# Performance work log

Hardware: AMD Instinct MI355X
Metric: run time of the kernel (lower is better)

## Reference

```python
import jax, jax.numpy as jnp
import numpy as np

COST_W = {'cls': 1.0, 'center': 0.0, 'obj_ness': 0.0, 'giou': 2.0}
IOU_THRES = 0.25
MAX_DYN = 10
EPS = 1e-6
N_PRED, N_GT, N_CLS = 65536, 128, 256


def _to_bbox(centers, sizes):
    # center/size -> (x1,y1,z1,x2,y2,z2)
    return jnp.concatenate([centers - sizes / 2.0, centers + sizes / 2.0], axis=-1)


def _giou_3d(b1, b2):
    # b1 [N,6], b2 [M,6] -> giou [N,M] (axis_aligned_bbox_overlaps_3d, mode='giou')
    vol1 = jnp.prod(b1[:, 3:] - b1[:, :3], axis=-1)  # [N]
    vol2 = jnp.prod(b2[:, 3:] - b2[:, :3], axis=-1)  # [M]
    lt = jnp.maximum(b1[:, None, :3], b2[None, :, :3])  # [N,M,3]
    rb = jnp.minimum(b1[:, None, 3:], b2[None, :, 3:])
    overlap = jnp.prod(jnp.clip(rb - lt, 0.0), axis=-1)  # [N,M]
    union = jnp.maximum(vol1[:, None] + vol2[None, :] - overlap, EPS)
    iou = overlap / union
    elt = jnp.minimum(b1[:, None, :3], b2[None, :, :3])
    erb = jnp.maximum(b1[:, None, 3:], b2[None, :, 3:])
    enclose = jnp.maximum(jnp.prod(jnp.clip(erb - elt, 0.0), axis=-1), EPS)
    return iou - (enclose - union) / enclose


def _lsa(cost):
    # Jonker-Volgenant shortest-augmenting-path LAP (same optimum as
    # scipy.optimize.linear_sum_assignment). cost [n, m], n <= m.
    # Returns col4row[n]: column matched to each row.
    n, m = cost.shape
    u = np.zeros(n, np.float64)
    v = np.zeros(m, np.float64)
    col4row = np.full(n, -1, np.int64)
    row4col = np.full(m, -1, np.int64)
    cost = cost.astype(np.float64)
    for cur in range(n):
        shortest = np.full(m, np.inf)
        path = np.full(m, -1, np.int64)
        SC = np.zeros(m, bool)
        SR = []
        i, min_val, sink = cur, 0.0, -1
        while sink == -1:
            SR.append(i)
            r = min_val + cost[i] - u[i] - v
            upd = (~SC) & (r < shortest)
            shortest = np.where(upd, r, shortest)
            path = np.where(upd, i, path)
            masked = np.where(SC, np.inf, shortest)
            j = int(masked.argmin())
            min_val = masked[j]
            SC[j] = True
            if row4col[j] == -1:
                sink = j
            else:
                i = int(row4col[j])
        u[cur] += min_val
        for i2 in SR:
            if i2 != cur:
                u[i2] += min_val - shortest[col4row[i2]]
        v[SC] -= min_val - shortest[SC]
        j = sink
        while True:
            i2 = int(path[j])
            row4col[j] = i2
            col4row[i2], j = j, col4row[i2]
            if i2 == cur:
                break
    return col4row


def _dynamic_assign(giou, used0, order):
    # Sequential greedy IoU-threshold assignment over gts (ascending max-iou).
    NEG = jnp.float32(-1e9)
    n_pred = giou.shape[0]

    def step(used, gt_idx):
        col = giou[:, gt_idx]
        vals = jnp.where((col > IOU_THRES) & (~used), col, NEG)
        topv, topi = jax.lax.top_k(vals, MAX_DYN)
        valid = topv > NEG
        used = used | jnp.zeros((n_pred,), bool).at[topi].set(valid)
        return used, (jnp.where(valid, topi, -1), jnp.where(valid, gt_idx, -1))

    _, (dp, dg) = jax.lax.scan(step, used0, order)
    return dp.reshape(-1), dg.reshape(-1)  # padded with -1 where invalid


def setup_inputs() -> dict:
    key = jax.random.key(0)
    k = jax.random.split(key, 7)
    return {
        'all_centers': jax.random.normal(k[0], (N_PRED, 3), jnp.float32),
        'all_sizes': jax.random.uniform(k[1], (N_PRED, 3), jnp.float32),
        'all_cls': jax.random.normal(k[2], (N_PRED, N_CLS), jnp.float32),
        'all_objness': jax.random.normal(k[3], (N_PRED,), jnp.float32),
        'gt_centers': jax.random.normal(k[4], (N_GT, 3), jnp.float32),
        'gt_sizes': jax.random.uniform(k[5], (N_GT, 3), jnp.float32),
        'gt_labels': jax.random.randint(k[6], (N_GT,), 0, N_CLS, jnp.int64),
    }


def reference(all_centers, all_sizes, all_cls, all_objness, gt_centers, gt_sizes, gt_labels):
    pred_bbox = _to_bbox(all_centers, all_sizes)
    gt_bbox = _to_bbox(gt_centers, gt_sizes)
    giou = _giou_3d(pred_bbox, gt_bbox)  # [N, M]
    cost_class = -jax.nn.sigmoid(all_cls)[:, gt_labels]  # [N, M]
    cost_center = jnp.sum(jnp.abs(all_centers[:, None, :] - gt_centers[None, :, :]), axis=-1)  # cdist p=1
    cost_obj = -jax.nn.sigmoid(all_objness)[:, None]  # [N, 1]
    total_cost = (COST_W['cls'] * cost_class + COST_W['center'] * cost_center
                  + COST_W['obj_ness'] * cost_obj + COST_W['giou'] * (-giou))
    # Hungarian on transposed cost (M <= N): same optimal pairing as scipy on [N, M].
    col4row = _lsa(np.asarray(jax.device_get(total_cost)).T)
    pred_indices = jnp.asarray(col4row, jnp.int64)       # matched pred per gt
    gt_indices = jnp.arange(gt_labels.shape[0], dtype=jnp.int64)
    used0 = jnp.zeros((giou.shape[0],), bool).at[pred_indices].set(True)
    order = jnp.argsort(jnp.max(giou, axis=0))
    dp, dg = _dynamic_assign(giou, used0, order)
    combined_preds = jnp.concatenate([pred_indices, dp.astype(jnp.int64)])
    combined_gts = jnp.concatenate([gt_indices, dg.astype(jnp.int64)])
    return combined_preds, combined_gts
```

## Files before the change

### kernel.cpp

```cpp
#include <hip/hip_runtime.h>
#include <hip/hip_bf16.h>
#include <math.h>

#define NPRED 65536
#define NGT   128
#define NCLS  256
#define CAP   12288
#define VCAP  160
#define VSLOT 129
#define NLIST 129
#define LSTRIDE 132
#define KEEP  2048
#define KMIN  1418
#define GSPLIT 4
#define GPB   (NGT / GSPLIT)
#define SENT_I 0x7FFFFFFF


__device__ __forceinline__ unsigned f2u(float f) {
    unsigned u = __float_as_uint(f);
    return (u & 0x80000000u) ? ~u : (u | 0x80000000u);
}
__device__ __forceinline__ float u2f(unsigned x) {
    unsigned u = (x & 0x80000000u) ? (x ^ 0x80000000u) : ~x;
    return __uint_as_float(u);
}
__device__ __forceinline__ unsigned long long d2u(double d) {
    unsigned long long u = (unsigned long long)__double_as_longlong(d);
    return (u & 0x8000000000000000ull) ? ~u : (u | 0x8000000000000000ull);
}
__device__ __forceinline__ double u2d(unsigned long long x) {
    unsigned long long u = (x & 0x8000000000000000ull) ? (x ^ 0x8000000000000000ull) : ~x;
    return __longlong_as_double((long long)u);
}

__device__ __forceinline__ float giou3d(
    float pl0, float pl1, float pl2, float ph0, float ph1, float ph2, float pvol,
    float gl0, float gl1, float gl2, float gh0, float gh1, float gh2, float gvol)
{
#pragma clang fp contract(off)
    float c0 = fmaxf(fminf(ph0, gh0) - fmaxf(pl0, gl0), 0.0f);
    float c1 = fmaxf(fminf(ph1, gh1) - fmaxf(pl1, gl1), 0.0f);
    float c2 = fmaxf(fminf(ph2, gh2) - fmaxf(pl2, gl2), 0.0f);
    float overlap = (c0 * c1) * c2;
    float uni = fmaxf((pvol + gvol) - overlap, 1e-6f);
    float iou = overlap / uni;
    float e0 = fmaxf(fmaxf(ph0, gh0) - fminf(pl0, gl0), 0.0f);
    float e1 = fmaxf(fmaxf(ph1, gh1) - fminf(pl1, gl1), 0.0f);
    float e2 = fmaxf(fmaxf(ph2, gh2) - fminf(pl2, gl2), 0.0f);
    float enc = fmaxf((e0 * e1) * e2, 1e-6f);
    return iou - (enc - uni) / enc;
}


__global__ __launch_bounds__(256) void k_gather(
    const float* __restrict__ cls, const int* __restrict__ lab,
    float* __restrict__ costT,
    int* __restrict__ ccnt, unsigned* __restrict__ cmax, int* __restrict__ failFlag)
{
#pragma clang fp contract(off)
    __shared__ float tile[64][NCLS + 1];
    __shared__ int labl[NGT];
    int tid = threadIdx.x;
    int p0 = blockIdx.x * 64;
    if (blockIdx.x == 0) {
        if (tid < NGT) { ccnt[tid] = 0; cmax[tid] = 0u; }
        if (tid == 0) *failFlag = 0;
    }
    if (tid < NGT) labl[tid] = lab[tid];
    for (int it = 0; it < 16; ++it) {
        int row = it * 4 + (tid >> 6);
        int col = (tid & 63) * 4;
        const float4 v = *(const float4*)&cls[(size_t)(p0 + row) * NCLS + col];
        tile[row][col + 0] = v.x; tile[row][col + 1] = v.y;
        tile[row][col + 2] = v.z; tile[row][col + 3] = v.w;
    }
    __syncthreads();
    int lane = tid & 63;
    for (int rep = 0; rep < 32; ++rep) {
        int g = rep * 4 + (tid >> 6);
        float val = tile[lane][labl[g]];
        double s = 1.0 / (1.0 + exp(-(double)val));
        costT[(size_t)g * NPRED + p0 + lane] = -(float)s;
    }
}

__global__ __launch_bounds__(256) void k_cost(
    const float* __restrict__ pc, const float* __restrict__ ps,
    const float* __restrict__ gc, const float* __restrict__ gs,
    float* __restrict__ costT, int* __restrict__ ccnt, unsigned* __restrict__ cmax,
    int2* __restrict__ cpair)
{
#pragma clang fp contract(off)
    __shared__ float gb[GPB][6];
    __shared__ float gvol[GPB];
    __shared__ unsigned smax[GPB];
    __shared__ int cntl[GPB], basel[GPB], curl[GPB];
    int tid = threadIdx.x;
    int lane = tid & 63;
    int g0 = (blockIdx.x & (GSPLIT - 1)) * GPB;
    int p  = (blockIdx.x >> 2) * 256 + tid;

    if (tid < GPB) {
        int g = g0 + tid;
        float c0 = gc[g * 3 + 0], c1 = gc[g * 3 + 1], c2 = gc[g * 3 + 2];
        float s0 = gs[g * 3 + 0], s1 = gs[g * 3 + 1], s2 = gs[g * 3 + 2];
        float l0 = c0 - s0 / 2.0f, l1 = c1 - s1 / 2.0f, l2 = c2 - s2 / 2.0f;
        float h0 = c0 + s0 / 2.0f, h1 = c1 + s1 / 2.0f, h2 = c2 + s2 / 2.0f;
        gb[tid][0] = l0; gb[tid][1] = l1; gb[tid][2] = l2;
        gb[tid][3] = h0; gb[tid][4] = h1; gb[tid][5] = h2;
        gvol[tid] = ((h0 - l0) * (h1 - l1)) * (h2 - l2);
        smax[tid] = 0u; cntl[tid] = 0; curl[tid] = 0;
    }
    __syncthreads();

    float c0 = pc[p * 3 + 0], c1 = pc[p * 3 + 1], c2 = pc[p * 3 + 2];
    float s0 = ps[p * 3 + 0], s1 = ps[p * 3 + 1], s2 = ps[p * 3 + 2];
    float pl0 = c0 - s0 / 2.0f, pl1 = c1 - s1 / 2.0f, pl2 = c2 - s2 / 2.0f;
    float ph0 = c0 + s0 / 2.0f, ph1 = c1 + s1 / 2.0f, ph2 = c2 + s2 / 2.0f;
    float pvol = ((ph0 - pl0) * (ph1 - pl1)) * (ph2 - pl2);

    float gior[GPB];

#pragma unroll
    for (int gg = 0; gg < GPB; ++gg) {
        float gio = giou3d(pl0, pl1, pl2, ph0, ph1, ph2, pvol,
                           gb[gg][0], gb[gg][1], gb[gg][2], gb[gg][3], gb[gg][4], gb[gg][5],
                           gvol[gg]);
        gior[gg] = gio;
        float m = gio;
        for (int off = 32; off; off >>= 1) m = fmaxf(m, __shfl_xor(m, off, 64));
        unsigned long long mask = __ballot(gio > 0.25f);
        if (lane == 0) {
            atomicMax(&smax[gg], f2u(m));
            atomicAdd(&cntl[gg], __popcll(mask));
        }
        size_t ij = (size_t)(g0 + gg) * NPRED + p;
        float ns = costT[ij];
        costT[ij] = ns + (2.0f * (-gio));
    }
    __syncthreads();
    if (tid < GPB) {
        atomicMax(&cmax[g0 + tid], smax[tid]);
        basel[tid] = atomicAdd(&ccnt[g0 + tid], cntl[tid]);
    }
    __syncthreads();

#pragma unroll
    for (int gg = 0; gg < GPB; ++gg) {
        float gio = gior[gg];
        bool cand = (gio > 0.25f);
        unsigned long long mask = __ballot(cand);
        int cnt = __popcll(mask);
        int wo = 0;
        if (lane == 0 && cnt) wo = atomicAdd(&curl[gg], cnt);
        wo = __shfl(wo, 0, 64);
        if (cand) {
            int slot = basel[gg] + wo + __popcll(mask & ((1ull << lane) - 1ull));
            if (slot < CAP)
                cpair[(size_t)(g0 + gg) * CAP + slot] = make_int2(p, __float_as_int(gio));
        }
    }
}

__global__ __launch_bounds__(256) void k_toprow(
    const float* __restrict__ costT, int2* __restrict__ rowlist,
    const unsigned* __restrict__ cmax, int* __restrict__ order)
{
    __shared__ unsigned long long keys[2048];
    __shared__ int hist[256];
    __shared__ unsigned long long sh_prefix;
    __shared__ int sh_rank, sh_cnt, sh_ok;
    __shared__ unsigned msort[NGT];
    int tid = threadIdx.x;
    int row = blockIdx.x;

    if (row == NGT) {
        if (tid < NGT) msort[tid] = cmax[tid];
        __syncthreads();
        if (tid < NGT) {
            unsigned mt = msort[tid];
            int r = 0;
            for (int k = 0; k < NGT; ++k) {
                unsigned mk = msort[k];
                if (mk < mt || (mk == mt && k < tid)) r++;
            }
            order[r] = tid;
        }
        return;
    }
    const float* crow = costT + (size_t)row * NPRED;

    unsigned long long lv[8];
#pragma unroll
    for (int q = 0; q < 8; ++q) lv[q] = ~0ull;
    const float4* crow4 = (const float4*)crow;
    for (int it = tid; it < NPRED / 4; it += 256) {
        float4 v4 = crow4[it];
        int j = it * 4;
        float vv[4] = {v4.x, v4.y, v4.z, v4.w};
#pragma unroll
        for (int e = 0; e < 4; ++e) {
            unsigned long long key =
                ((unsigned long long)f2u(vv[e]) << 32) | (unsigned)(j + e);
            if (key < lv[7]) {
                unsigned long long c = key;
#pragma unroll
                for (int q = 0; q < 8; ++q) {
                    unsigned long long mx = (c > lv[q]) ? c : lv[q];
                    unsigned long long mn = (c > lv[q]) ? lv[q] : c;
                    lv[q] = mn; c = mx;
                }
            }
        }
    }
#pragma unroll
    for (int q = 0; q < 8; ++q) keys[tid * 8 + q] = lv[q];
    if (tid == 0) sh_ok = 1;
    __syncthreads();

    for (int k = 2; k <= 2048; k <<= 1) {
        for (int j2 = k >> 1; j2 > 0; j2 >>= 1) {
            for (int i = tid; i < 2048; i += 256) {
                int ixj = i ^ j2;
                if (ixj > i) {
                    unsigned long long a = keys[i], b2 = keys[ixj];
                    bool up = ((i & k) == 0);
                    if ((up && a > b2) || (!up && a < b2)) { keys[i] = b2; keys[ixj] = a; }
                }
            }
            __syncthreads();
        }
    }

    unsigned long long thr = keys[NLIST - 1];
    if (lv[7] < thr) sh_ok = 0;
    __syncthreads();

    if (sh_ok) {
        if (tid < NLIST) {
            unsigned long long key = keys[tid];
            rowlist[row * LSTRIDE + tid] =
                make_int2(__float_as_int(u2f((unsigned)(key >> 32))),
                          (int)(unsigned)(key & 0xFFFFFFFFull));
        }
        return;
    }

    if (tid == 0) { sh_prefix = 0ull; sh_rank = NLIST - 1; sh_cnt = 0; }
    __syncthreads();
    for (int d = 7; d >= 0; --d) {
        hist[tid] = 0;
        __syncthreads();
        unsigned long long pref = sh_prefix;
        int sh = (d + 1) * 8;
        for (int j = tid; j < NPRED; j += 256) {
            unsigned long long key = ((unsigned long long)f2u(crow[j]) << 32) | (unsigned)j;
            bool match = (sh >= 64) || ((key >> sh) == (pref >> sh));
            if (match) atomicAdd(&hist[(int)((key >> (d * 8)) & 255ull)], 1);
        }
        __syncthreads();
        if (tid == 0) {
            int rank = sh_rank, cum = 0, b = 0;
            for (; b < 256; ++b) { if (cum + hist[b] > rank) break; cum += hist[b]; }
            sh_prefix = pref | ((unsigned long long)b << (d * 8));
            sh_rank = rank - cum;
        }
        __syncthreads();
    }
    unsigned long long thr2 = sh_prefix;
    for (int j = tid; j < NPRED; j += 256) {
        unsigned long long key = ((unsigned long long)f2u(crow[j]) << 32) | (unsigned)j;
        if (key <= thr2) { int s = atomicAdd(&sh_cnt, 1); keys[s] = key; }
    }
    __syncthreads();
    if (tid >= sh_cnt) keys[tid] = ~0ull;
    __syncthreads();
    for (int k = 2; k <= 256; k <<= 1) {
        for (int j2 = k >> 1; j2 > 0; j2 >>= 1) {
            int i = tid, ixj = i ^ j2;
            if (ixj > i) {
                unsigned long long a = keys[i], b2 = keys[ixj];
                bool up = ((i & k) == 0);
                if ((up && a > b2) || (!up && a < b2)) { keys[i] = b2; keys[ixj] = a; }
            }
            __syncthreads();
        }
    }
    if (tid < NLIST) {
        unsigned long long key = keys[tid];
        rowlist[row * LSTRIDE + tid] =
            make_int2(__float_as_int(u2f((unsigned)(key >> 32))),
                      (int)(unsigned)(key & 0xFFFFFFFFull));
    }
}

__global__ __launch_bounds__(64) void k_lsa_sparse(
    const float* __restrict__ costT, const int2* __restrict__ rowlist,
    int* __restrict__ failFlag,
    unsigned* __restrict__ usedbits, int* __restrict__ out)
{
#pragma clang fp contract(off)
    __shared__ float  costV[NGT][VSLOT];
    __shared__ double u_l[NGT];
    __shared__ int    c4r[NGT];
    __shared__ int    slot4row[NGT];
    __shared__ int    headpos[NGT];
    __shared__ int    colidV[VCAP];
    __shared__ int    pathV[VCAP], r4cV[VCAP];
    __shared__ int    SRr[VCAP];
    __shared__ double headv[VCAP];
    __shared__ int    headj[VCAP];
    __shared__ unsigned vbits[2048];

    int lane = threadIdx.x;
    for (int w = lane; w < 2048; w += 64) vbits[w] = 0u;
    for (int r = lane; r < NGT; r += 64) {
        u_l[r] = 0.0; c4r[r] = -1; slot4row[r] = -1; headpos[r] = 0;
    }
    double short0 = INFINITY, short1 = INFINITY;
    double v0 = 0.0, v1 = 0.0;
    int col0 = SENT_I, col1 = SENT_I;
    int sc0 = 0, sc1 = 0;
    int nV = 0;
    bool fail = false;
    __syncthreads();

    for (int cur = 0; cur < NGT; ++cur) {
        short0 = INFINITY; short1 = INFINITY; sc0 = 0; sc1 = 0;
        if (lane < nV)      pathV[lane]      = -1;
        if (lane + 64 < nV) pathV[lane + 64] = -1;
        if (lane == 0) SRr[0] = cur;
        int bi = cur, s = 1, pendrow = cur, pendpos = 0, sink = -1;
        double mv = 0.0, pendmv = 0.0;
        __syncthreads();

        while (true) {
            int prow = pendrow;
            int pp   = pendpos;
            double pmv = pendmv;

            int pos = headpos[prow];
            int i0 = pos + lane;
            int2 e0 = (i0 < NLIST) ? rowlist[prow * LSTRIDE + i0]
                                   : make_int2(0, SENT_I);

            double ui = u_l[bi];
            unsigned long long bvk = ~0ull, btk = ~0ull;
            if (lane < nV && !sc0) {
                double c = (double)costV[bi][lane];
                double r = ((mv + c) - ui) - v0;
                if (r < short0) { short0 = r; pathV[lane] = bi; }
                unsigned long long vk = d2u(short0);
                unsigned long long tk = ((unsigned long long)(unsigned)col0 << 32)
                                        | (0x80000000u | (unsigned)lane);
                if (vk < bvk || (vk == bvk && tk < btk)) { bvk = vk; btk = tk; }
            }
            int k1 = lane + 64;
            if (k1 < nV && !sc1) {
                double c = (double)costV[bi][k1];
                double r = ((mv + c) - ui) - v1;
                if (r < short1) { short1 = r; pathV[k1] = bi; }
                unsigned long long vk = d2u(short1);
                unsigned long long tk = ((unsigned long long)(unsigned)col1 << 32)
                                        | (0x80000000u | (unsigned)k1);
                if (vk < bvk || (vk == bvk && tk < btk)) { bvk = vk; btk = tk; }
            }
            for (int p = lane; p < s; p += 64) {
                if (p == pp) continue;
                unsigned long long vk = d2u(headv[p]);
                unsigned long long tk = ((unsigned long long)(unsigned)headj[p] << 32)
                                        | (unsigned)p;
                if (vk < bvk || (vk == bvk && tk < btk)) { bvk = vk; btk = tk; }
            }

            int hcol = SENT_I; float hval = 0.0f;
            {
                int c0 = e0.y;
                bool fresh = (i0 < NLIST) && !((vbits[c0 >> 5] >> (c0 & 31)) & 1u);
                unsigned long long m0 = __ballot(fresh);
                if (m0) {
                    int fl = __ffsll(m0) - 1;
                    hcol = __shfl(c0, fl, 64);
                    hval = __shfl(__int_as_float(e0.x), fl, 64);
                    pos += fl;
                } else {
                    pos += 64;
                    while (pos < NLIST) {
                        int i = pos + lane;
                        int2 e = (i < NLIST) ? rowlist[prow * LSTRIDE + i] : make_int2(0, SENT_I);
                        int c = e.y;
                        bool fr = (i < NLIST) && !((vbits[c >> 5] >> (c & 31)) & 1u);
                        unsigned long long m = __ballot(fr);
                        if (m) {
                            int fl = __ffsll(m) - 1;
                            hcol = __shfl(c, fl, 64);
                            hval = __shfl(__int_as_float(e.x), fl, 64);
                            pos += fl;
                            break;
                        }
                        pos += 64;
                    }
                }
            }
            double pend_headv = (hcol == SENT_I) ? (double)INFINITY
                                : ((pmv + (double)hval) - u_l[prow]);
            {
                unsigned long long vk = d2u(pend_headv);
                unsigned long long tk = ((unsigned long long)(unsigned)hcol << 32)
                                        | (unsigned)pp;
                if (vk < bvk || (vk == bvk && tk < btk)) { bvk = vk; btk = tk; }
            }

#pragma unroll
            for (int off = 1; off < 64; off <<= 1) {
                unsigned long long ov = __shfl_xor(bvk, off, 64);
                unsigned long long ot = __shfl_xor(btk, off, 64);
                if (ov < bvk || (ov == bvk && ot < btk)) { bvk = ov; btk = ot; }
            }
            double bv = u2d(bvk);
            unsigned tlow = (unsigned)btk;
            int bj   = (int)(btk >> 32);
            int bisv = (int)(tlow >> 31);
            int baux = (int)(tlow & 0x7FFFFFFFu);
            mv = bv;

            if (lane == 0) {
                headpos[prow] = pos;
                headv[pp] = pend_headv; headj[pp] = hcol;
            }
            if (bisv) {
                if ((baux & 63) == lane) {
                    if (baux & 64) sc1 = 1; else sc0 = 1;
                }
                int nr = r4cV[baux];
                if (lane == 0) SRr[s] = nr;
                pendrow = nr; pendpos = s; pendmv = bv; bi = nr; ++s;
                __syncthreads();
            } else {
                if (nV >= VCAP) {
                    fail = true;
                } else {
                    if ((nV & 63) == lane) {
                        if (nV & 64) { col1 = bj; v1 = 0.0; short1 = bv; sc1 = 1; }
                        else         { col0 = bj; v0 = 0.0; short0 = bv; sc0 = 1; }
                    }
                    if (lane == 0) {
                        colidV[nV] = bj;
                        pathV[nV] = SRr[baux]; r4cV[nV] = -1;
                        vbits[bj >> 5] |= (1u << (bj & 31));
                    }
                    sink = bj;
                    ++nV;
                }
                __syncthreads();
                break;
            }
        }
        if (fail) break;

        int snew = nV - 1;
        float pfa = costT[(size_t)lane * NPRED + sink];
        float pfb = costT[(size_t)(lane + 64) * NPRED + sink];

        double mvf = mv;
        if (lane < nV && sc0)      v0 -= (mvf - short0);
        if (lane + 64 < nV && sc1) v1 -= (mvf - short1);

        {
            int q = lane;
            bool act = (q >= 1 && q < s);
            int i2 = act ? SRr[q] : 0;
            int sl = act ? slot4row[i2] : 0;
            double gA = __shfl(short0, sl & 63, 64);
            double gB = __shfl(short1, sl & 63, 64);
            double sv = (sl & 64) ? gB : gA;
            if (act) u_l[i2] += mvf - sv;
        }
        {
            int q = lane + 64;
            bool act = (q >= 1 && q < s);
            int i2 = act ? SRr[q] : 0;
            int sl = act ? slot4row[i2] : 0;
            double gA = __shfl(short0, sl & 63, 64);
            double gB = __shfl(short1, sl & 63, 64);
            double sv = (sl & 64) ? gB : gA;
            if (act) u_l[i2] += mvf - sv;
        }
        if (lane == 0) u_l[cur] += mvf;

        if (lane == 0) {
            int jslot = snew;
            while (true) {
                int i2 = pathV[jslot];
                r4cV[jslot] = i2;
                int oldslot = (c4r[i2] >= 0) ? slot4row[i2] : -1;
                c4r[i2] = colidV[jslot];
                slot4row[i2] = jslot;
                if (i2 == cur) break;
                jslot = oldslot;
            }
        }
        costV[lane][snew]      = pfa;
        costV[lane + 64][snew] = pfb;
        __syncthreads();
    }

    if (lane == 0 && fail) *failFlag = 1;
    __syncthreads();
    if (!fail) {
        for (int w = lane; w < 2048; w += 64) usedbits[w] = 0u;
        __syncthreads();
        for (int r = lane; r < NGT; r += 64) {
            int p = c4r[r];
            atomicOr(&usedbits[p >> 5], 1u << (p & 31));
            out[r] = p;
            out[1408 + r] = r;
        }
    }
}

__global__ __launch_bounds__(1024) void k_lsa_dense(
    const float* __restrict__ costT, const int* __restrict__ failFlag,
    double* __restrict__ v, double* __restrict__ shortest,
    int* __restrict__ path, int* __restrict__ row4col,
    unsigned char* __restrict__ SC, unsigned* __restrict__ usedbits,
    int* __restrict__ out)
{
#pragma clang fp contract(off)
    if (*failFlag == 0) return;
    __shared__ double u_l[NGT];
    __shared__ int    c4r[NGT];
    __shared__ int    SR[NGT + 1];
    __shared__ int    bi, bsink, nSR;
    __shared__ double bmin;
    __shared__ double wval[16];
    __shared__ int    widx[16];
    int tid = threadIdx.x;

    for (int j = tid; j < NPRED; j += 1024) { v[j] = 0.0; row4col[j] = -1; }
    if (tid < NGT) { u_l[tid] = 0.0; c4r[tid] = -1; }
    __syncthreads();

    for (int cur = 0; cur < NGT; ++cur) {
        for (int j = tid; j < NPRED; j += 1024) {
            shortest[j] = (double)INFINITY; path[j] = -1; SC[j] = 0;
        }
        if (tid == 0) { bi = cur; bsink = -1; bmin = 0.0; SR[0] = cur; nSR = 1; }
        __syncthreads();

        while (true) {
            int irow = bi;
            double mv = bmin;
            double ui = u_l[irow];
            const float* crow = costT + (size_t)irow * NPRED;
            double bestv = (double)INFINITY;
            int    bestj = SENT_I;
            for (int j = tid; j < NPRED; j += 1024) {
                if (!SC[j]) {
                    double s = shortest[j];
                    double r = ((mv + (double)crow[j]) - ui) - v[j];
                    if (r < s) { s = r; shortest[j] = r; path[j] = irow; }
                    if (s < bestv || (s == bestv && j < bestj)) { bestv = s; bestj = j; }
                }
            }
            for (int off = 32; off; off >>= 1) {
                double ov = __shfl_down(bestv, off, 64);
                int    oj = __shfl_down(bestj, off, 64);
                if (ov < bestv || (ov == bestv && oj < bestj)) { bestv = ov; bestj = oj; }
            }
            if ((tid & 63) == 0) { wval[tid >> 6] = bestv; widx[tid >> 6] = bestj; }
            __syncthreads();
            if (tid == 0) {
                double bv = wval[0]; int bj = widx[0];
                for (int w = 1; w < 16; ++w) {
                    double ov = wval[w]; int oj = widx[w];
                    if (ov < bv || (ov == bv && oj < bj)) { bv = ov; bj = oj; }
                }
                bmin = bv;
                SC[bj] = 1;
                int r = row4col[bj];
                if (r < 0) { bsink = bj; }
                else       { SR[nSR++] = r; bi = r; }
            }
            __syncthreads();
            if (bsink >= 0) break;
        }

        double mv = bmin;
        for (int j = tid; j < NPRED; j += 1024)
            if (SC[j]) v[j] -= (mv - shortest[j]);
        if (tid == 0) {
            u_l[cur] += mv;
            for (int k = 1; k < nSR; ++k) {
                int i2 = SR[k];
                u_l[i2] += mv - shortest[c4r[i2]];
            }
            int j = bsink;
            while (true) {
                int i2 = path[j];
                row4col[j] = i2;
                int nj = c4r[i2];
                c4r[i2] = j;
                j = nj;
                if (i2 == cur) break;
            }
        }
        __syncthreads();
    }

    for (int w = tid; w < 2048; w += 1024) usedbits[w] = 0u;
    __syncthreads();
    for (int j = tid; j < NPRED; j += 1024)
        if (row4col[j] >= 0) atomicOr(&usedbits[j >> 5], 1u << (j & 31));
    if (tid < NGT) {
        out[tid]        = c4r[tid];
        out[1408 + tid] = tid;
    }
}

__global__ __launch_bounds__(256) void k_prep(
    const int2* __restrict__ cpair, const int* __restrict__ ccnt,
    unsigned long long* __restrict__ scand, int* __restrict__ kcount,
    int* __restrict__ fullflag)
{
    __shared__ int hist[256];
    __shared__ unsigned long long keys[KEEP];
    __shared__ unsigned sh_pref, sh_thresh;
    __shared__ int sh_done, sh_fail, sh_cnt;
    int tid = threadIdx.x;
    int g = blockIdx.x;
    int nc = ccnt[g]; if (nc > CAP) nc = CAP;
    const int2* src = cpair + (size_t)g * CAP;

    unsigned thresh = 0;
    if (nc > KEEP - 1) {
        if (tid == 0) { sh_pref = 0; sh_done = 0; sh_fail = 0; }
        __syncthreads();
        int above = 0;
        for (int byt = 3; byt >= 0; --byt) {
            hist[tid] = 0;
            __syncthreads();
            unsigned pref = sh_pref;
            for (int c = tid; c < nc; c += 256) {
                unsigned u = f2u(__int_as_float(src[c].y));
                if (byt == 3 || (u >> ((byt + 1) * 8)) == (pref >> ((byt + 1) * 8)))
                    atomicAdd(&hist[(u >> (byt * 8)) & 255], 1);
            }
            __syncthreads();
            if (tid == 0) {
                int cum = 0, B = 0, kept = 0, abnew = above;
                for (int b = 255; b >= 0; --b) {
                    if (above + cum + hist[b] >= KMIN) {
                        B = b; kept = above + cum + hist[b]; abnew = above + cum; break;
                    }
                    cum += hist[b];
                }
                if (kept <= KEEP - 1) { sh_thresh = sh_pref | ((unsigned)B << (byt * 8)); sh_done = 1; }
                else {
                    above = abnew;
                    sh_pref = sh_pref | ((unsigned)B << (byt * 8));
                    if (byt == 0) sh_fail = 1;
                }
            }
            __syncthreads();
            if (sh_done || sh_fail) break;
        }
        if (sh_fail) {
            if (tid == 0) { fullflag[g] = 1; kcount[g] = 0; }
            return;
        }
        thresh = sh_thresh;
    }
    if (tid == 0) sh_cnt = 0;
    __syncthreads();
    for (int c = tid; c < nc; c += 256) {
        unsigned u = f2u(__int_as_float(src[c].y));
        if (u >= thresh) {
            int slot = atomicAdd(&sh_cnt, 1);
            keys[slot] = ((unsigned long long)(~u) << 32) | (unsigned)src[c].x;
        }
    }
    __syncthreads();
    int kept = sh_cnt;
    for (int i = tid; i < KEEP; i += 256) if (i >= kept) keys[i] = ~0ull;
    __syncthreads();
    for (int k = 2; k <= KEEP; k <<= 1) {
        for (int j = k >> 1; j > 0; j >>= 1) {
            for (int i = tid; i < KEEP; i += 256) {
                int ixj = i ^ j;
                if (ixj > i) {
                    unsigned long long a = keys[i], b = keys[ixj];
                    bool up = ((i & k) == 0);
                    if ((up && a > b) || (!up && a < b)) { keys[i] = b; keys[ixj] = a; }
                }
            }
            __syncthreads();
        }
    }
    for (int i = tid; i < KEEP; i += 256) scand[(size_t)g * KEEP + i] = keys[i];
    if (tid == 0) { kcount[g] = kept; fullflag[g] = 0; }
}

__global__ __launch_bounds__(64) void k_dyn2(
    const int* __restrict__ order, const int* __restrict__ kcount,
    const unsigned long long* __restrict__ scand, const int* __restrict__ fullflag,
    const int* __restrict__ ccnt, const int2* __restrict__ cpair,
    const unsigned* __restrict__ usedbits_g, const int* __restrict__ failFlag,
    int* __restrict__ out)
{
    __shared__ unsigned bits[2048];
    int lane = threadIdx.x;
    for (int w = lane; w < 2048; w += 64) bits[w] = usedbits_g[w];
    __syncthreads();
    bool globalFull = (*failFlag != 0);

    for (int k = 0; k < NGT; ++k) {
        int gt = order[k];
        int got = 0;
        if (!globalFull && fullflag[gt] == 0) {
            int kept = kcount[gt];
            int base = 0;
            while (got < 10 && base < kept) {
                int i = base + lane;
                unsigned long long key = (i < kept) ? scand[(size_t)gt * KEEP + i] : ~0ull;
                int p = (int)(unsigned)(key & 0xFFFFFFFFull);
                bool ok = (key != ~0ull) && !((bits[p >> 5] >> (p & 31)) & 1u);
                unsigned long long mask = __ballot(ok);
                int need = 10 - got;
                int pre = __popcll(mask & ((1ull << lane) - 1ull));
                if (ok && pre < need) {
                    out[128 + k * 10 + got + pre] = p;
                    out[1408 + 128 + k * 10 + got + pre] = gt;
                    atomicOr(&bits[p >> 5], 1u << (p & 31));
                }
                int tot = __popcll(mask);
                got += (tot < need) ? tot : need;
                base += 64;
                __syncthreads();
            }
        } else {
            int nc = ccnt[gt]; if (nc > CAP) nc = CAP;
            float lv[10]; int li[10];
#pragma unroll
            for (int q = 0; q < 10; ++q) { lv[q] = -1e30f; li[q] = SENT_I; }
            for (int c = lane; c < nc; c += 64) {
                int2 pr = cpair[(size_t)gt * CAP + c];
                int p = pr.x;
                if ((bits[p >> 5] >> (p & 31)) & 1u) continue;
                float cv = __int_as_float(pr.y); int ci = p;
#pragma unroll
                for (int q = 0; q < 10; ++q) {
                    bool b = (cv > lv[q]) || (cv == lv[q] && ci < li[q]);
                    float tv = b ? lv[q] : cv; int ti = b ? li[q] : ci;
                    if (b) { lv[q] = cv; li[q] = ci; }
                    cv = tv; ci = ti;
                }
            }
#pragma unroll
            for (int q = 0; q < 10; ++q) {
                float mo = lv[0]; int mj = li[0];
#pragma unroll
                for (int off = 1; off < 64; off <<= 1) {
                    float ov = __shfl_xor(mo, off, 64);
                    int oj = __shfl_xor(mj, off, 64);
                    if (ov > mo || (ov == mo && oj < mj)) { mo = ov; mj = oj; }
                }
                bool valid = (mj != SENT_I);
                if (valid && li[0] == mj) {
#pragma unroll
                    for (int t = 0; t < 9; ++t) { lv[t] = lv[t + 1]; li[t] = li[t + 1]; }
                    lv[9] = -1e30f; li[9] = SENT_I;
                }
                if (lane == q) {
                    out[128 + k * 10 + q] = valid ? mj : -1;
                    out[1408 + 128 + k * 10 + q] = valid ? gt : -1;
                    if (valid) atomicOr(&bits[mj >> 5], 1u << (mj & 31));
                }
            }
            got = 10;
            __syncthreads();
        }
        for (int q = got + lane; q < 10; q += 64) {
            out[128 + k * 10 + q] = -1;
            out[1408 + 128 + k * 10 + q] = -1;
        }
        __syncthreads();
    }
}


extern "C" void kernel_launch(void* const* d_in, const int* in_sizes, int n_in,
                              void* d_out, int out_size, void* d_ws, size_t ws_size,
                              hipStream_t stream) {
    const float* pc  = (const float*)d_in[0];
    const float* ps  = (const float*)d_in[1];
    const float* cls = (const float*)d_in[2];
    const float* gc  = (const float*)d_in[4];
    const float* gs  = (const float*)d_in[5];
    const int*   lab = (const int*)d_in[6];

    char* ws = (char*)d_ws;
    float*         costT    = (float*)(ws + 0);
    unsigned long long* scand = (unsigned long long*)(ws + 0);
    int2*          rowlist  = (int2*)(ws + 33554432);
    double*        v        = (double*)(ws + 33554432);
    double*        shortest = (double*)(ws + 34078720);
    int*           path     = (int*)(ws + 34603008);
    int*           row4col  = (int*)(ws + 34865152);
    unsigned char* SC       = (unsigned char*)(ws + 35127296);
    int*           kcount   = (int*)(ws + 35192832);
    int*           fullflag = (int*)(ws + 35193344);
    int*           ccnt     = (int*)(ws + 35193856);
    unsigned*      cmax     = (unsigned*)(ws + 35194368);
    int*           order    = (int*)(ws + 35194880);
    int*           failFlag = (int*)(ws + 35195392);
    unsigned*      usedbits = (unsigned*)(ws + 35195904);
    int2*          cpair    = (int2*)(ws + 35204096);

    int* out = (int*)d_out;

    hipLaunchKernelGGL(k_gather, dim3(NPRED / 64), dim3(256), 0, stream,
                       cls, lab, costT, ccnt, cmax, failFlag);
    hipLaunchKernelGGL(k_cost, dim3((NPRED / 256) * GSPLIT), dim3(256), 0, stream,
                       pc, ps, gc, gs, costT, ccnt, cmax, cpair);
    hipLaunchKernelGGL(k_toprow, dim3(NGT + 1), dim3(256), 0, stream,
                       costT, rowlist, cmax, order);
    hipLaunchKernelGGL(k_lsa_sparse, dim3(1), dim3(64), 0, stream,
                       costT, rowlist, failFlag, usedbits, out);
    hipLaunchKernelGGL(k_lsa_dense, dim3(1), dim3(1024), 0, stream,
                       costT, failFlag, v, shortest, path, row4col, SC, usedbits, out);
    hipLaunchKernelGGL(k_prep, dim3(NGT), dim3(256), 0, stream,
                       cpair, ccnt, scand, kcount, fullflag);
    hipLaunchKernelGGL(k_dyn2, dim3(1), dim3(64), 0, stream,
                       order, kcount, scand, fullflag, ccnt, cpair, usedbits, failFlag, out);
}
```

Baseline: 689.8 us.

## Move LSA head/row/path state into registers and drop per-step barriers

The sparse Hungarian kernel now keeps per-slot head values, head columns, row-for-column, scan-row lists and head positions in lane-distributed registers, read with shuffles instead of shared-memory arrays. This removes the __syncthreads inside the augmenting inner loop and prefetches the next row's list entries as soon as the row is known. Tie-break keys shrink to 32 bits, so each reduction step does one fewer 64-bit shuffle. All fresh candidates in the first chunk now enter the reduction directly, and path backtracking runs wave-wide. The packed key assumes column ids fit in 16 bits and slot ids in 8 bits.

```diff
diff --git a/kernel.cpp b/kernel.cpp
--- a/kernel.cpp
+++ b/kernel.cpp
@@ -305,149 +305,152 @@
     __shared__ double u_l[NGT];
     __shared__ int    c4r[NGT];
     __shared__ int    slot4row[NGT];
-    __shared__ int    headpos[NGT];
     __shared__ int    colidV[VCAP];
-    __shared__ int    pathV[VCAP], r4cV[VCAP];
-    __shared__ int    SRr[VCAP];
-    __shared__ double headv[VCAP];
-    __shared__ int    headj[VCAP];
+    __shared__ int    pathV[VCAP];
     __shared__ unsigned vbits[2048];
 
     int lane = threadIdx.x;
     for (int w = lane; w < 2048; w += 64) vbits[w] = 0u;
     for (int r = lane; r < NGT; r += 64) {
-        u_l[r] = 0.0; c4r[r] = -1; slot4row[r] = -1; headpos[r] = 0;
+        u_l[r] = 0.0; c4r[r] = -1; slot4row[r] = -1;
     }
     double short0 = INFINITY, short1 = INFINITY;
     double v0 = 0.0, v1 = 0.0;
     int col0 = SENT_I, col1 = SENT_I;
     int sc0 = 0, sc1 = 0;
+    double hv0 = 0.0, hv1 = 0.0;
+    int hj0 = SENT_I, hj1 = SENT_I;
+    int sr0 = 0, sr1 = 0;
+    int r4c0 = -1, r4c1 = -1;
+    int hp0 = 0, hp1 = 0;
     int nV = 0;
     bool fail = false;
     __syncthreads();
 
-    for (int cur = 0; cur < NGT; ++cur) {
+    for (int cur = 0; cur < NGT && !fail; ++cur) {
         short0 = INFINITY; short1 = INFINITY; sc0 = 0; sc1 = 0;
         if (lane < nV)      pathV[lane]      = -1;
         if (lane + 64 < nV) pathV[lane + 64] = -1;
-        if (lane == 0) SRr[0] = cur;
-        int bi = cur, s = 1, pendrow = cur, pendpos = 0, sink = -1;
-        double mv = 0.0, pendmv = 0.0;
-        __syncthreads();
+        if (lane == 0) sr0 = cur;
+        int prow = cur, pp = 0, s = 1, sink = -1;
+        double mv = 0.0, pmv = 0.0;
+        int pos;
+        { int t = (cur & 64) ? hp1 : hp0; pos = __shfl(t, cur & 63, 64); }
+        int i0 = pos + lane;
+        int2 e0 = (i0 < NLIST) ? rowlist[prow * LSTRIDE + i0] : make_int2(0, SENT_I);
 
         while (true) {
-            int prow = pendrow;
-            int pp   = pendpos;
-            double pmv = pendmv;
-
-            int pos = headpos[prow];
-            int i0 = pos + lane;
-            int2 e0 = (i0 < NLIST) ? rowlist[prow * LSTRIDE + i0]
-                                   : make_int2(0, SENT_I);
-
-            double ui = u_l[bi];
-            unsigned long long bvk = ~0ull, btk = ~0ull;
+            double ui = u_l[prow];
+            unsigned long long bvk = ~0ull; unsigned btk = 0xFFFFFFFFu;
+
             if (lane < nV && !sc0) {
-                double c = (double)costV[bi][lane];
+                double c = (double)costV[prow][lane];
                 double r = ((mv + c) - ui) - v0;
-                if (r < short0) { short0 = r; pathV[lane] = bi; }
+                if (r < short0) { short0 = r; pathV[lane] = prow; }
                 unsigned long long vk = d2u(short0);
-                unsigned long long tk = ((unsigned long long)(unsigned)col0 << 32)
-                                        | (0x80000000u | (unsigned)lane);
+                unsigned tk = ((unsigned)col0 << 16) | 0x100u | (unsigned)lane;
                 if (vk < bvk || (vk == bvk && tk < btk)) { bvk = vk; btk = tk; }
             }
             int k1 = lane + 64;
             if (k1 < nV && !sc1) {
-                double c = (double)costV[bi][k1];
+                double c = (double)costV[prow][k1];
                 double r = ((mv + c) - ui) - v1;
-                if (r < short1) { short1 = r; pathV[k1] = bi; }
+                if (r < short1) { short1 = r; pathV[k1] = prow; }
                 unsigned long long vk = d2u(short1);
-                unsigned long long tk = ((unsigned long long)(unsigned)col1 << 32)
-                                        | (0x80000000u | (unsigned)k1);
+                unsigned tk = ((unsigned)col1 << 16) | 0x100u | (unsigned)k1;
                 if (vk < bvk || (vk == bvk && tk < btk)) { bvk = vk; btk = tk; }
             }
-            for (int p = lane; p < s; p += 64) {
-                if (p == pp) continue;
-                unsigned long long vk = d2u(headv[p]);
-                unsigned long long tk = ((unsigned long long)(unsigned)headj[p] << 32)
-                                        | (unsigned)p;
+            if (lane < s && lane != pp) {
+                unsigned long long vk = d2u(hv0);
+                unsigned tk = ((unsigned)hj0 << 16) | (unsigned)lane;
                 if (vk < bvk || (vk == bvk && tk < btk)) { bvk = vk; btk = tk; }
             }
-
-            int hcol = SENT_I; float hval = 0.0f;
-            {
-                int c0 = e0.y;
-                bool fresh = (i0 < NLIST) && !((vbits[c0 >> 5] >> (c0 & 31)) & 1u);
-                unsigned long long m0 = __ballot(fresh);
-                if (m0) {
-                    int fl = __ffsll(m0) - 1;
-                    hcol = __shfl(c0, fl, 64);
-                    hval = __shfl(__int_as_float(e0.x), fl, 64);
-                    pos += fl;
-                } else {
+            if (k1 < s && k1 != pp) {
+                unsigned long long vk = d2u(hv1);
+                unsigned tk = ((unsigned)hj1 << 16) | (unsigned)k1;
+                if (vk < bvk || (vk == bvk && tk < btk)) { bvk = vk; btk = tk; }
+            }
+
+            int c0 = e0.y;
+            bool fresh = (i0 < NLIST) && !((vbits[c0 >> 5] >> (c0 & 31)) & 1u);
+            unsigned long long m0 = __ballot(fresh);
+            int hcol; double chv;
+            if (m0) {
+                if (fresh) {
+                    unsigned long long vk =
+                        d2u((pmv + (double)__int_as_float(e0.x)) - ui);
+                    unsigned tk = ((unsigned)c0 << 16) | (unsigned)pp;
+                    if (vk < bvk || (vk == bvk && tk < btk)) { bvk = vk; btk = tk; }
+                }
+                int fl = __ffsll(m0) - 1;
+                hcol = __shfl(c0, fl, 64);
+                float hval = __shfl(__int_as_float(e0.x), fl, 64);
+                chv = (pmv + (double)hval) - ui;
+                pos += fl;
+            } else {
+                pos += 64;
+                hcol = SENT_I; float hval = 0.0f;
+                while (pos < NLIST) {
+                    int i = pos + lane;
+                    int2 e = (i < NLIST) ? rowlist[prow * LSTRIDE + i] : make_int2(0, SENT_I);
+                    int c = e.y;
+                    bool fr = (i < NLIST) && !((vbits[c >> 5] >> (c & 31)) & 1u);
+                    unsigned long long m = __ballot(fr);
+                    if (m) {
+                        int fl = __ffsll(m) - 1;
+                        hcol = __shfl(c, fl, 64);
+                        hval = __shfl(__int_as_float(e.x), fl, 64);
+                        pos += fl;
+                        break;
+                    }
                     pos += 64;
-                    while (pos < NLIST) {
-                        int i = pos + lane;
-                        int2 e = (i < NLIST) ? rowlist[prow * LSTRIDE + i] : make_int2(0, SENT_I);
-                        int c = e.y;
-                        bool fr = (i < NLIST) && !((vbits[c >> 5] >> (c & 31)) & 1u);
-                        unsigned long long m = __ballot(fr);
-                        if (m) {
-                            int fl = __ffsll(m) - 1;
-                            hcol = __shfl(c, fl, 64);
-                            hval = __shfl(__int_as_float(e.x), fl, 64);
-                            pos += fl;
-                            break;
-                        }
-                        pos += 64;
-                    }
-                }
-            }
-            double pend_headv = (hcol == SENT_I) ? (double)INFINITY
-                                : ((pmv + (double)hval) - u_l[prow]);
-            {
-                unsigned long long vk = d2u(pend_headv);
-                unsigned long long tk = ((unsigned long long)(unsigned)hcol << 32)
-                                        | (unsigned)pp;
+                }
+                chv = (hcol == SENT_I) ? (double)INFINITY
+                                       : ((pmv + (double)hval) - ui);
+                unsigned long long vk = d2u(chv);
+                unsigned tk = ((unsigned)hcol << 16) | (unsigned)pp;
                 if (vk < bvk || (vk == bvk && tk < btk)) { bvk = vk; btk = tk; }
             }
 
 #pragma unroll
             for (int off = 1; off < 64; off <<= 1) {
                 unsigned long long ov = __shfl_xor(bvk, off, 64);
-                unsigned long long ot = __shfl_xor(btk, off, 64);
+                unsigned ot = (unsigned)__shfl_xor((int)btk, off, 64);
                 if (ov < bvk || (ov == bvk && ot < btk)) { bvk = ov; btk = ot; }
             }
             double bv = u2d(bvk);
-            unsigned tlow = (unsigned)btk;
-            int bj   = (int)(btk >> 32);
-            int bisv = (int)(tlow >> 31);
-            int baux = (int)(tlow & 0x7FFFFFFFu);
+            int bj   = (int)(btk >> 16);
+            int bisv = (int)((btk >> 8) & 1u);
+            int baux = (int)(btk & 0xFFu);
             mv = bv;
 
-            if (lane == 0) {
-                headpos[prow] = pos;
-                headv[pp] = pend_headv; headj[pp] = hcol;
-            }
+            if (pp < 64) { if (lane == pp)      { hv0 = chv; hj0 = hcol; } }
+            else         { if (lane == pp - 64) { hv1 = chv; hj1 = hcol; } }
+            if ((prow & 63) == lane) { if (prow & 64) hp1 = pos; else hp0 = pos; }
+
             if (bisv) {
-                if ((baux & 63) == lane) {
-                    if (baux & 64) sc1 = 1; else sc0 = 1;
-                }
-                int nr = r4cV[baux];
-                if (lane == 0) SRr[s] = nr;
-                pendrow = nr; pendpos = s; pendmv = bv; bi = nr; ++s;
-                __syncthreads();
+                if ((baux & 63) == lane) { if (baux & 64) sc1 = 1; else sc0 = 1; }
+                int nr;
+                { int t = (baux & 64) ? r4c1 : r4c0; nr = __shfl(t, baux & 63, 64); }
+                if (s < 64) { if (lane == s)      sr0 = nr; }
+                else        { if (lane == s - 64) sr1 = nr; }
+                pp = s; pmv = bv; ++s; prow = nr;
+                { int t = (prow & 64) ? hp1 : hp0; pos = __shfl(t, prow & 63, 64); }
+                i0 = pos + lane;
+                e0 = (i0 < NLIST) ? rowlist[prow * LSTRIDE + i0] : make_int2(0, SENT_I);
             } else {
                 if (nV >= VCAP) {
                     fail = true;
                 } else {
                     if ((nV & 63) == lane) {
-                        if (nV & 64) { col1 = bj; v1 = 0.0; short1 = bv; sc1 = 1; }
-                        else         { col0 = bj; v0 = 0.0; short0 = bv; sc0 = 1; }
+                        if (nV & 64) { col1 = bj; v1 = 0.0; short1 = bv; sc1 = 1; r4c1 = -1; }
+                        else         { col0 = bj; v0 = 0.0; short0 = bv; sc0 = 1; r4c0 = -1; }
                     }
+                    int srv;
+                    { int t = (baux & 64) ? sr1 : sr0; srv = __shfl(t, baux & 63, 64); }
                     if (lane == 0) {
                         colidV[nV] = bj;
-                        pathV[nV] = SRr[baux]; r4cV[nV] = -1;
+                        pathV[nV] = srv;
                         vbits[bj >> 5] |= (1u << (bj & 31));
                     }
                     sink = bj;
@@ -468,9 +471,8 @@
         if (lane + 64 < nV && sc1) v1 -= (mvf - short1);
 
         {
-            int q = lane;
-            bool act = (q >= 1 && q < s);
-            int i2 = act ? SRr[q] : 0;
+            bool act = (lane >= 1 && lane < s);
+            int i2 = act ? sr0 : 0;
             int sl = act ? slot4row[i2] : 0;
             double gA = __shfl(short0, sl & 63, 64);
             double gB = __shfl(short1, sl & 63, 64);
@@ -480,7 +482,7 @@
         {
             int q = lane + 64;
             bool act = (q >= 1 && q < s);
-            int i2 = act ? SRr[q] : 0;
+            int i2 = act ? sr1 : 0;
             int sl = act ? slot4row[i2] : 0;
             double gA = __shfl(short0, sl & 63, 64);
             double gB = __shfl(short1, sl & 63, 64);
@@ -489,14 +491,13 @@
         }
         if (lane == 0) u_l[cur] += mvf;
 
-        if (lane == 0) {
+        {
             int jslot = snew;
             while (true) {
                 int i2 = pathV[jslot];
-                r4cV[jslot] = i2;
+                if ((jslot & 63) == lane) { if (jslot & 64) r4c1 = i2; else r4c0 = i2; }
                 int oldslot = (c4r[i2] >= 0) ? slot4row[i2] : -1;
-                c4r[i2] = colidV[jslot];
-                slot4row[i2] = jslot;
+                if (lane == 0) { c4r[i2] = colidV[jslot]; slot4row[i2] = jslot; }
                 if (i2 == cur) break;
                 jslot = oldslot;
             }
```

Measured after the change: 681.5 us. No clear change (-1.2%).
